# Kernel tuning notes

Hardware: AMD Instinct MI355X
Metric: run time of the kernel (lower is better)

Reference implementation:

```python
import jax, jax.numpy as jnp
import numpy as np

B, S, SEQ_PER = 1, 4, 512            # batch, num_sequences (tickers), per-stock length (seq_len+1)
L = S * SEQ_PER                      # total sequence length = 2048
D_MODEL, NHEAD, HEAD_DIM = 1024, 16, 64
KVC, QC, ROPE = 512, 512, 32
D_FF = 4096
H2 = NHEAD * 2                       # differential attention sub-heads
HD2 = HEAD_DIM // 2
RD2 = ROPE // 2
SCALING = float(((HEAD_DIM + ROPE) // 2) ** -0.5)
LAMBDA_INIT = float(0.8 - 0.6 * np.exp(-0.3 * 0))  # depth = 0
EPS = float(np.finfo(np.float32).eps)              # torch RMSNorm default eps


def rmsnorm(x, w, eps=EPS):
    return x * jax.lax.rsqrt(jnp.mean(x * x, axis=-1, keepdims=True) + eps) * w


def rope_rotate(x, fr, fi):
    # x: (B, S, T, H2, RD2) viewed as complex pairs along last dim; fr/fi: (T, RD2//2)
    a = x[..., 0::2]
    b = x[..., 1::2]
    cr = fr[None, None, :, None, :]
    ci = fi[None, None, :, None, :]
    ya = a * cr - b * ci
    yb = a * ci + b * cr
    return jnp.stack([ya, yb], axis=-1).reshape(x.shape)


def setup_inputs() -> dict:
    key = jax.random.key(0)
    ks = jax.random.split(key, 16)
    x = jax.random.normal(ks[0], (B, L, D_MODEL), dtype=jnp.float32)
    # rotary frequencies for the seq_per_stock-1 rotated positions, rope_dim//4 complex freqs
    t = np.arange(SEQ_PER - 1, dtype=np.float32)
    inv = 1.0 / (10000.0 ** (np.arange(ROPE // 4, dtype=np.float32) / (ROPE // 4)))
    ang = t[:, None] * inv[None, :]
    freqs_r = jnp.asarray(np.cos(ang), dtype=jnp.float32)
    freqs_i = jnp.asarray(np.sin(ang), dtype=jnp.float32)
    # block-tiled causal mask: causal(seq_per) tiled (S,S) -> (1,1,L,L); True = masked
    causal = np.triu(np.ones((SEQ_PER, SEQ_PER), dtype=bool), k=1)
    mask = jnp.asarray(np.tile(causal, (S, S))[None, None])
    w = lambda k, shape: (jax.random.normal(k, shape, dtype=jnp.float32) * 0.02)
    return {
        "x": x, "freqs_r": freqs_r, "freqs_i": freqs_i, "mask": mask,
        "kv_down_w": w(ks[1], (D_MODEL, KVC + ROPE)),
        "q_down_w": w(ks[2], (D_MODEL, QC)),
        "kv_up_w": w(ks[3], (KVC, NHEAD * HEAD_DIM * 2)),
        "q_up_w": w(ks[4], (QC, NHEAD * (HEAD_DIM + ROPE))),
        "kv_norm_w": jnp.ones((KVC,), jnp.float32),
        "q_norm_w": jnp.ones((QC,), jnp.float32),
        "o_w": w(ks[5], (NHEAD * HEAD_DIM, D_MODEL)),
        "lambda_q1": jax.random.normal(ks[6], (HD2,), jnp.float32) * 0.1,
        "lambda_k1": jax.random.normal(ks[7], (HD2,), jnp.float32) * 0.1,
        "lambda_q2": jax.random.normal(ks[8], (HD2,), jnp.float32) * 0.1,
        "lambda_k2": jax.random.normal(ks[9], (HD2,), jnp.float32) * 0.1,
        "head_norm_w": jnp.ones((HEAD_DIM,), jnp.float32),
        "norm1_w": jnp.ones((D_MODEL,), jnp.float32),
        "norm2_w": jnp.ones((D_MODEL,), jnp.float32),
        "ff_in_w": w(ks[10], (D_MODEL, D_FF * 2)),
        "ff_out_w": w(ks[11], (D_FF, D_MODEL)),
    }


def reference(x, freqs_r, freqs_i, mask, kv_down_w, q_down_w, kv_up_w, q_up_w,
              kv_norm_w, q_norm_w, o_w, lambda_q1, lambda_k1, lambda_q2, lambda_k2,
              head_norm_w, norm1_w, norm2_w, ff_in_w, ff_out_w):
    b, sl, _ = x.shape
    # ---- attention sublayer ----
    h = rmsnorm(x, norm1_w)
    ckv = h @ kv_down_w                                   # (B,L,KVC+ROPE)
    c_kv, k_rope = ckv[..., :KVC], ckv[..., KVC:]
    kv = rmsnorm(c_kv, kv_norm_w) @ kv_up_w               # (B,L,NHEAD*HEAD_DIM*2)
    kv = kv.reshape(b, sl, NHEAD, HEAD_DIM * 2)
    k = kv[..., :HEAD_DIM].reshape(b, sl, H2, HD2)
    v = kv[..., HEAD_DIM:]                                # (B,L,NHEAD,HEAD_DIM)
    q_full = rmsnorm(h @ q_down_w, q_norm_w) @ q_up_w
    q_full = q_full.reshape(b, sl, NHEAD, HEAD_DIM + ROPE)
    q = q_full[..., :HEAD_DIM].reshape(b, sl, H2, HD2)
    q_rope = q_full[..., HEAD_DIM:].reshape(b, sl, H2, RD2)
    k_rope = jnp.broadcast_to(k_rope[:, :, None, :], (b, sl, NHEAD, ROPE)).reshape(b, sl, H2, RD2)
    # per-stock RoPE: first token of each stock left unrotated
    qr = q_rope.reshape(b, S, SEQ_PER, H2, RD2)
    kr = k_rope.reshape(b, S, SEQ_PER, H2, RD2)
    q_rot = rope_rotate(qr[:, :, 1:], freqs_r, freqs_i)
    k_rot = rope_rotate(kr[:, :, 1:], freqs_r, freqs_i)
    q_rope = jnp.concatenate([qr[:, :, :1], q_rot], axis=2).reshape(b, sl, H2, RD2)
    k_rope = jnp.concatenate([kr[:, :, :1], k_rot], axis=2).reshape(b, sl, H2, RD2)
    qh = jnp.concatenate([q, q_rope], axis=-1).transpose(0, 2, 1, 3)  # (B,H2,L,HD2+RD2)
    kh = jnp.concatenate([k, k_rope], axis=-1).transpose(0, 2, 1, 3)
    vh = v.transpose(0, 2, 1, 3)                                      # (B,NHEAD,L,HEAD_DIM)
    a = jnp.einsum('bhqd,bhkd->bhqk', qh, kh) * SCALING               # (B,H2,L,L)
    abs_a = jnp.where(mask, -1e9, jnp.abs(a))
    p = jnp.sign(a) * jax.nn.softmax(abs_a, axis=-1)
    lam = (jnp.exp(jnp.sum(lambda_k1 * lambda_q1)) - jnp.exp(jnp.sum(lambda_k2 * lambda_q2))
           + LAMBDA_INIT)
    p = p.reshape(b, NHEAD, 2, sl, sl)
    a1, a2 = p[:, :, 0], p[:, :, 1]
    g = jnp.mean(a1, axis=-2, keepdims=True)                          # (B,NHEAD,1,L)
    attn_w = a1 - lam * a2 + g * lam
    attn_w = jnp.where(mask, 0.0, attn_w)
    out = jnp.einsum('bhqk,bhkd->bhqd', attn_w, vh)                   # (B,NHEAD,L,HEAD_DIM)
    out = rmsnorm(out.transpose(0, 2, 1, 3), head_norm_w, eps=1e-5)
    out = out.reshape(b, sl, NHEAD * HEAD_DIM) @ o_w
    x = x + out
    # ---- SwiGLU FFN sublayer ----
    h2 = rmsnorm(x, norm2_w)
    uv = h2 @ ff_in_w
    u, g2 = uv[..., :D_FF], uv[..., D_FF:]
    x = x + (u * jax.nn.silu(g2)) @ ff_out_w
    return x
```

## Files before the change

kernel.cpp:

```cpp
#include <hip/hip_runtime.h>
#include <math.h>

#define LQ 2048
#define SCALING 0.14433756729740643f
#define FEPS 1.1920928955078125e-07f

typedef unsigned short u16;
typedef __attribute__((ext_vector_type(8))) short bf16x8;
typedef __attribute__((ext_vector_type(4))) float f32x4;

#define MFMA16(a, b, c) __builtin_amdgcn_mfma_f32_16x16x32_bf16((a), (b), (c), 0, 0, 0)

__device__ __forceinline__ u16 f2b(float x) {
  union { float f; unsigned u; } v; v.f = x;
  return (u16)((v.u + 0x7FFFu + ((v.u >> 16) & 1u)) >> 16);
}
__device__ __forceinline__ float b2f(u16 b) {
  union { unsigned u; float f; } v; v.u = ((unsigned)b) << 16;
  return v.f;
}

__global__ __launch_bounds__(256) void prep_weights_kernel(
    const float* __restrict__ kvd, u16* __restrict__ kvd_h, u16* __restrict__ kvd_l,
    const float* __restrict__ qd,  u16* __restrict__ qd_h,  u16* __restrict__ qd_l,
    const float* __restrict__ kvu, u16* __restrict__ kvu_h, u16* __restrict__ kvu_l,
    const float* __restrict__ qu,  u16* __restrict__ qu_h,  u16* __restrict__ qu_l,
    const float* __restrict__ ow,  u16* __restrict__ ow_t,
    const float* __restrict__ ffi, u16* __restrict__ ffi_t,
    const float* __restrict__ ffo, u16* __restrict__ ffo_t) {
  __shared__ float tile[32][33];
  int id = blockIdx.x;
  const float* W; u16* Whi; u16* Wlo = nullptr; int K, N, bx, by;
  if (id < 8192) {
    W = ffi; Whi = ffi_t; K = 1024; N = 8192; bx = id % 256; by = id / 256;
  } else if (id < 8192 + 4096) {
    id -= 8192;
    W = ffo; Whi = ffo_t; K = 4096; N = 1024; bx = id % 32; by = id / 32;
  } else if (id < 12288 + 1024) {
    id -= 12288;
    W = ow; Whi = ow_t; K = 1024; N = 1024; bx = id % 32; by = id / 32;
  } else if (id < 13312 + 544) {
    id -= 13312;
    W = kvd; Whi = kvd_h; Wlo = kvd_l; K = 1024; N = 544; bx = id % 17; by = id / 17;
  } else if (id < 13856 + 512) {
    id -= 13856;
    W = qd; Whi = qd_h; Wlo = qd_l; K = 1024; N = 512; bx = id % 16; by = id / 16;
  } else if (id < 14368 + 1024) {
    id -= 14368;
    W = kvu; Whi = kvu_h; Wlo = kvu_l; K = 512; N = 2048; bx = id % 64; by = id / 64;
  } else {
    id -= 15392;
    W = qu; Whi = qu_h; Wlo = qu_l; K = 512; N = 1536; bx = id % 48; by = id / 48;
  }

  int n0 = bx * 32, k0 = by * 32;
  int tx = threadIdx.x, ty = threadIdx.y;
  for (int i = ty; i < 32; i += 8) {
    int k = k0 + i, n = n0 + tx;
    tile[i][tx] = (k < K && n < N) ? W[(size_t)k * N + n] : 0.f;
  }
  __syncthreads();
  for (int i = ty; i < 32; i += 8) {
    int n = n0 + i, k = k0 + tx;
    if (n < N && k < K) {
      float xv = tile[tx][i];
      u16 hi = f2b(xv);
      Whi[(size_t)n * K + k] = hi;
      if (Wlo) Wlo[(size_t)n * K + k] = f2b(xv - b2f(hi));
    }
  }
}

template <int BF16OUT>
__global__ __launch_bounds__(256) void rmsnorm_kernel(
    const float* __restrict__ x, const float* __restrict__ w, void* __restrict__ outv,
    int cols, int in_stride, float eps) {
  const int row = blockIdx.x;
  const float* xr = x + (size_t)row * in_stride;
  float ss = 0.f;
  for (int c = threadIdx.x; c < cols; c += 256) { float v = xr[c]; ss = fmaf(v, v, ss); }
#pragma unroll
  for (int off = 32; off > 0; off >>= 1) ss += __shfl_xor(ss, off);
  __shared__ float red[4];
  if ((threadIdx.x & 63) == 0) red[threadIdx.x >> 6] = ss;
  __syncthreads();
  float tot = red[0] + red[1] + red[2] + red[3];
  float sc = 1.f / sqrtf(tot / (float)cols + eps);
  for (int c = threadIdx.x; c < cols; c += 256) {
    float v = xr[c] * sc * w[c];
    if (BF16OUT) ((u16*)outv)[(size_t)row * cols + c] = f2b(v);
    else ((float*)outv)[(size_t)row * cols + c] = v;
  }
}

__global__ __launch_bounds__(256) void rmsnorm_split_kernel(
    const float* __restrict__ x, const float* __restrict__ w,
    u16* __restrict__ hi_out, u16* __restrict__ lo_out,
    int cols, int in_stride, float eps) {
  const int row = blockIdx.x;
  const float* xr = x + (size_t)row * in_stride;
  float ss = 0.f;
  for (int c = threadIdx.x; c < cols; c += 256) { float v = xr[c]; ss = fmaf(v, v, ss); }
#pragma unroll
  for (int off = 32; off > 0; off >>= 1) ss += __shfl_xor(ss, off);
  __shared__ float red[4];
  if ((threadIdx.x & 63) == 0) red[threadIdx.x >> 6] = ss;
  __syncthreads();
  float tot = red[0] + red[1] + red[2] + red[3];
  float sc = 1.f / sqrtf(tot / (float)cols + eps);
  for (int c = threadIdx.x; c < cols; c += 256) {
    float v = xr[c] * sc * w[c];
    u16 hi = f2b(v);
    hi_out[(size_t)row * cols + c] = hi;
    lo_out[(size_t)row * cols + c] = f2b(v - b2f(hi));
  }
}

__global__ __launch_bounds__(256) void rmsnorm_split2_kernel(
    const float* __restrict__ in0, const float* __restrict__ w0,
    u16* __restrict__ hi0, u16* __restrict__ lo0, int stride0,
    const float* __restrict__ in1, const float* __restrict__ w1,
    u16* __restrict__ hi1, u16* __restrict__ lo1, int stride1) {
  int row = blockIdx.x;
  const float* xr; const float* w; u16* ho; u16* lo;
  if (row < 2048) {
    xr = in0 + (size_t)row * stride0; w = w0;
    ho = hi0 + (size_t)row * 512; lo = lo0 + (size_t)row * 512;
  } else {
    row -= 2048;
    xr = in1 + (size_t)row * stride1; w = w1;
    ho = hi1 + (size_t)row * 512; lo = lo1 + (size_t)row * 512;
  }
  float ss = 0.f;
  for (int c = threadIdx.x; c < 512; c += 256) { float v = xr[c]; ss = fmaf(v, v, ss); }
#pragma unroll
  for (int off = 32; off > 0; off >>= 1) ss += __shfl_xor(ss, off);
  __shared__ float red[4];
  if ((threadIdx.x & 63) == 0) red[threadIdx.x >> 6] = ss;
  __syncthreads();
  float tot = red[0] + red[1] + red[2] + red[3];
  float sc = 1.f / sqrtf(tot / 512.f + FEPS);
  for (int c = threadIdx.x; c < 512; c += 256) {
    float v = xr[c] * sc * w[c];
    u16 hi = f2b(v);
    ho[c] = hi;
    lo[c] = f2b(v - b2f(hi));
  }
}

__global__ __launch_bounds__(256) void gemm_split(
    const u16* __restrict__ Ahi, const u16* __restrict__ Alo,
    const u16* __restrict__ Bhi, const u16* __restrict__ Blo,
    float* __restrict__ C, int M, int N, int K) {
  __shared__ u16 Ah[64][72];
  __shared__ u16 Al[64][72];
  __shared__ u16 Bh[64][72];
  __shared__ u16 Bl[64][72];

  const int t = threadIdx.x;
  const int lane = t & 63;
  const int wv = t >> 6;
  const int wr = (wv >> 1) * 32;
  const int wc = (wv & 1) * 32;
  const int bm = blockIdx.y * 64;
  const int bn = blockIdx.x * 64;
  const int lr = t >> 2;
  const int lc = (t & 3) * 16;
  const int rsel = lane & 15;
  const int ksel = 8 * (lane >> 4);

  const u16* Ahrow = Ahi + (size_t)(bm + lr) * K + lc;
  const u16* Alrow = Alo + (size_t)(bm + lr) * K + lc;
  const bool bval = (bn + lr) < N;
  const u16* Bhrow = Bhi + (size_t)(bn + lr) * K + lc;
  const u16* Blrow = Blo + (size_t)(bn + lr) * K + lc;

  f32x4 acc[2][2] = {};

  for (int kt = 0; kt < K; kt += 64) {
    uint4 ah0 = *(const uint4*)(Ahrow + kt);
    uint4 ah1 = *(const uint4*)(Ahrow + kt + 8);
    uint4 al0 = *(const uint4*)(Alrow + kt);
    uint4 al1 = *(const uint4*)(Alrow + kt + 8);
    uint4 bh0 = {0, 0, 0, 0}, bh1 = {0, 0, 0, 0}, bl0 = {0, 0, 0, 0}, bl1 = {0, 0, 0, 0};
    if (bval) {
      bh0 = *(const uint4*)(Bhrow + kt); bh1 = *(const uint4*)(Bhrow + kt + 8);
      bl0 = *(const uint4*)(Blrow + kt); bl1 = *(const uint4*)(Blrow + kt + 8);
    }
    __syncthreads();
    *(uint4*)&Ah[lr][lc] = ah0; *(uint4*)&Ah[lr][lc + 8] = ah1;
    *(uint4*)&Al[lr][lc] = al0; *(uint4*)&Al[lr][lc + 8] = al1;
    *(uint4*)&Bh[lr][lc] = bh0; *(uint4*)&Bh[lr][lc + 8] = bh1;
    *(uint4*)&Bl[lr][lc] = bl0; *(uint4*)&Bl[lr][lc + 8] = bl1;
    __syncthreads();
#pragma unroll
    for (int ks = 0; ks < 2; ++ks) {
      const int ko = ks * 32 + ksel;
      bf16x8 a0h = *(const bf16x8*)&Ah[wr + rsel][ko];
      bf16x8 a1h = *(const bf16x8*)&Ah[wr + 16 + rsel][ko];
      bf16x8 a0l = *(const bf16x8*)&Al[wr + rsel][ko];
      bf16x8 a1l = *(const bf16x8*)&Al[wr + 16 + rsel][ko];
      bf16x8 b0h = *(const bf16x8*)&Bh[wc + rsel][ko];
      bf16x8 b1h = *(const bf16x8*)&Bh[wc + 16 + rsel][ko];
      bf16x8 b0l = *(const bf16x8*)&Bl[wc + rsel][ko];
      bf16x8 b1l = *(const bf16x8*)&Bl[wc + 16 + rsel][ko];
      acc[0][0] = MFMA16(a0h, b0h, acc[0][0]);
      acc[0][0] = MFMA16(a0h, b0l, acc[0][0]);
      acc[0][0] = MFMA16(a0l, b0h, acc[0][0]);
      acc[0][1] = MFMA16(a0h, b1h, acc[0][1]);
      acc[0][1] = MFMA16(a0h, b1l, acc[0][1]);
      acc[0][1] = MFMA16(a0l, b1h, acc[0][1]);
      acc[1][0] = MFMA16(a1h, b0h, acc[1][0]);
      acc[1][0] = MFMA16(a1h, b0l, acc[1][0]);
      acc[1][0] = MFMA16(a1l, b0h, acc[1][0]);
      acc[1][1] = MFMA16(a1h, b1h, acc[1][1]);
      acc[1][1] = MFMA16(a1h, b1l, acc[1][1]);
      acc[1][1] = MFMA16(a1l, b1h, acc[1][1]);
    }
  }
  const int r0 = (lane >> 4) * 4;
#pragma unroll
  for (int fm = 0; fm < 2; ++fm)
#pragma unroll
    for (int fn = 0; fn < 2; ++fn)
#pragma unroll
      for (int j = 0; j < 4; ++j) {
        int row = bm + wr + fm * 16 + r0 + j;
        int col = bn + wc + fn * 16 + rsel;
        if (col < N) C[(size_t)row * N + col] = acc[fm][fn][j];
      }
}

template <int GATED, int ADDX>
__global__ __launch_bounds__(256) void gemm_kernel(
    const u16* __restrict__ A, const u16* __restrict__ Bt, const float* __restrict__ X,
    float* __restrict__ C, u16* __restrict__ Cg, int M, int N, int K) {
  __shared__ u16 As[64][72];
  __shared__ u16 Bs[64][72];
  __shared__ u16 Bs2[GATED ? 64 : 1][72];

  const int t = threadIdx.x;
  const int lane = t & 63;
  const int wv = t >> 6;
  const int wr = (wv >> 1) * 32;
  const int wc = (wv & 1) * 32;
  const int bm = blockIdx.y * 64;
  const int bn = blockIdx.x * 64;
  const int lr = t >> 2;
  const int lc = (t & 3) * 16;
  const int rsel = lane & 15;
  const int ksel = 8 * (lane >> 4);

  const u16* Arow = A + (size_t)(bm + lr) * K + lc;
  const u16* Brow = Bt + (size_t)(bn + lr) * K + lc;
  const u16* Brow2 = Bt + (size_t)(4096 + bn + lr) * K + lc;

  f32x4 acc[2][2] = {};
  f32x4 accg[2][2] = {};

  for (int kt = 0; kt < K; kt += 64) {
    uint4 a0 = *(const uint4*)(Arow + kt);
    uint4 a1 = *(const uint4*)(Arow + kt + 8);
    uint4 b0 = *(const uint4*)(Brow + kt);
    uint4 b1 = *(const uint4*)(Brow + kt + 8);
    uint4 c0 = {0, 0, 0, 0}, c1 = {0, 0, 0, 0};
    if (GATED) { c0 = *(const uint4*)(Brow2 + kt); c1 = *(const uint4*)(Brow2 + kt + 8); }
    __syncthreads();
    *(uint4*)&As[lr][lc] = a0; *(uint4*)&As[lr][lc + 8] = a1;
    *(uint4*)&Bs[lr][lc] = b0; *(uint4*)&Bs[lr][lc + 8] = b1;
    if (GATED) { *(uint4*)&Bs2[lr][lc] = c0; *(uint4*)&Bs2[lr][lc + 8] = c1; }
    __syncthreads();
#pragma unroll
    for (int ks = 0; ks < 2; ++ks) {
      const int ko = ks * 32 + ksel;
      bf16x8 af0 = *(const bf16x8*)&As[wr + rsel][ko];
      bf16x8 af1 = *(const bf16x8*)&As[wr + 16 + rsel][ko];
      bf16x8 bf0 = *(const bf16x8*)&Bs[wc + rsel][ko];
      bf16x8 bf1 = *(const bf16x8*)&Bs[wc + 16 + rsel][ko];
      acc[0][0] = MFMA16(af0, bf0, acc[0][0]);
      acc[0][1] = MFMA16(af0, bf1, acc[0][1]);
      acc[1][0] = MFMA16(af1, bf0, acc[1][0]);
      acc[1][1] = MFMA16(af1, bf1, acc[1][1]);
      if (GATED) {
        bf16x8 cf0 = *(const bf16x8*)&Bs2[wc + rsel][ko];
        bf16x8 cf1 = *(const bf16x8*)&Bs2[wc + 16 + rsel][ko];
        accg[0][0] = MFMA16(af0, cf0, accg[0][0]);
        accg[0][1] = MFMA16(af0, cf1, accg[0][1]);
        accg[1][0] = MFMA16(af1, cf0, accg[1][0]);
        accg[1][1] = MFMA16(af1, cf1, accg[1][1]);
      }
    }
  }
  const int r0 = (lane >> 4) * 4;
#pragma unroll
  for (int fm = 0; fm < 2; ++fm)
#pragma unroll
    for (int fn = 0; fn < 2; ++fn)
#pragma unroll
      for (int j = 0; j < 4; ++j) {
        int row = bm + wr + fm * 16 + r0 + j;
        int col = bn + wc + fn * 16 + rsel;
        size_t o = (size_t)row * N + col;
        if (!GATED) {
          float v = acc[fm][fn][j];
          if (ADDX) v += X[o];
          C[o] = v;
        } else {
          float u = acc[fm][fn][j], g = accg[fm][fn][j];
          float sv = g / (1.f + __expf(-g));
          Cg[o] = f2b(u * sv);
        }
      }
}

__global__ __launch_bounds__(256) void build_mid_kernel(
    const float* __restrict__ qfull, const float* __restrict__ kv,
    const float* __restrict__ ckv, const float* __restrict__ fr,
    const float* __restrict__ fi, u16* __restrict__ qhi, u16* __restrict__ qlo,
    u16* __restrict__ khi, u16* __restrict__ klo, u16* __restrict__ vt,
    const float* __restrict__ lq1, const float* __restrict__ lk1,
    const float* __restrict__ lq2, const float* __restrict__ lk2,
    float* __restrict__ lamp) {
  __shared__ u16 tile[64][65];
  int id = blockIdx.x;
  if (id < 16384) {
    const int q = id & 2047;
    const int h2 = ((id >> 11) << 2) + (threadIdx.x >> 6);
    const int d = threadIdx.x & 63;
    const int hh = h2 >> 1, s = h2 & 1;
    const float* row = qfull + (size_t)q * 1536 + hh * 96;
    float val;
    if (d < 32) {
      val = row[s * 32 + d];
    } else if (d < 48) {
      int r = d - 32;
      int pos = q & 511;
      const float* rp = row + 64 + s * 16;
      if (pos == 0) val = rp[r];
      else {
        int j = r >> 1;
        float cr = fr[(pos - 1) * 8 + j], ci = fi[(pos - 1) * 8 + j];
        float a = rp[2 * j], b = rp[2 * j + 1];
        val = (r & 1) ? (a * ci + b * cr) : (a * cr - b * ci);
      }
    } else val = 0.f;
    u16 hi = f2b(val);
    qhi[((size_t)h2 * LQ + q) * 64 + d] = hi;
    qlo[((size_t)h2 * LQ + q) * 64 + d] = f2b(val - b2f(hi));
    return;
  }
  id -= 16384;
  if (id < 16384) {
    const int kp = id & 2047;
    const int h2 = ((id >> 11) << 2) + (threadIdx.x >> 6);
    const int d = threadIdx.x & 63;
    const int hh = h2 >> 1, s = h2 & 1;
    float val;
    if (d < 32) {
      val = kv[(size_t)kp * 2048 + hh * 128 + s * 32 + d];
    } else if (d < 48) {
      int r = d - 32;
      int pos = kp & 511;
      const float* rp = ckv + (size_t)kp * 544 + 512 + s * 16;
      if (pos == 0) val = rp[r];
      else {
        int j = r >> 1;
        float cr = fr[(pos - 1) * 8 + j], ci = fi[(pos - 1) * 8 + j];
        float a = rp[2 * j], b = rp[2 * j + 1];
        val = (r & 1) ? (a * ci + b * cr) : (a * cr - b * ci);
      }
    } else val = 0.f;
    u16 hi = f2b(val);
    khi[((size_t)h2 * LQ + kp) * 64 + d] = hi;
    klo[((size_t)h2 * LQ + kp) * 64 + d] = f2b(val - b2f(hi));
    return;
  }
  id -= 16384;
  if (id < 512) {
    int h = id >> 5, k0 = (id & 31) * 64;
    int t = threadIdx.x;
    int d = t & 63, kr = t >> 6;
#pragma unroll
    for (int i = 0; i < 16; ++i) {
      int k = kr + i * 4;
      tile[k][d] = f2b(kv[(size_t)(k0 + k) * 2048 + h * 128 + 64 + d]);
    }
    __syncthreads();
    int kk = t & 63, dr = t >> 6;
#pragma unroll
    for (int i = 0; i < 16; ++i) {
      int d2 = dr + i * 4;
      vt[((size_t)h * 64 + d2) * LQ + k0 + kk] = tile[kk][d2];
    }
    return;
  }
  int t = threadIdx.x;
  if (t < 32) {
    float a = lq1[t] * lk1[t], b = lq2[t] * lk2[t];
#pragma unroll
    for (int off = 1; off < 32; off <<= 1) { a += __shfl_xor(a, off); b += __shfl_xor(b, off); }
    if (t == 0) lamp[0] = expf(a) - expf(b) + 0.2f;
  }
}

#define SCORE6(z, a0h, a1h, a0l, a1l, ph, pl)                         \
  {                                                                   \
    bf16x8 bh0 = *(const bf16x8*)(ph), bh1 = *(const bf16x8*)((ph) + 32); \
    bf16x8 bl0 = *(const bf16x8*)(pl), bl1 = *(const bf16x8*)((pl) + 32); \
    z = MFMA16(a0h, bh0, z); z = MFMA16(a1h, bh1, z);                 \
    z = MFMA16(a0h, bl0, z); z = MFMA16(a1h, bl1, z);                 \
    z = MFMA16(a0l, bh0, z); z = MFMA16(a1l, bh1, z);                 \
  }

__global__ __launch_bounds__(256) void attn_z_kernel(
    const u16* __restrict__ qhi, const u16* __restrict__ khi,
    float* __restrict__ zp) {
  __shared__ u16 Kh[2][64][72];

  const int bid = blockIdx.x;
  const int c = 7 - (bid >> 9);
  const int r = bid & 511;
  const int h2 = r & 31;
  const int qtIdx = (r >> 5) & 3;
  const int s = r >> 7;
  const int qt = qtIdx * 8 + c;
  const int qb = qt * 64;
  const int t = threadIdx.x;
  const int lane = t & 63, wv = t >> 6;
  const int rsel = lane & 15, grp = lane >> 4, ksel = 8 * grp;
  const int qrow = qb + wv * 16;

  const size_t qoff = ((size_t)h2 * LQ + qrow + rsel) * 64 + ksel;
  bf16x8 aq0h = *(const bf16x8*)(qhi + qoff), aq1h = *(const bf16x8*)(qhi + qoff + 32);
  const u16* kh = khi + (size_t)h2 * LQ * 64;

  const int srow = t >> 2;
  const int scol = (t & 3) * 16;

  int qm[4];
  float Z[4] = {0.f, 0.f, 0.f, 0.f};
#pragma unroll
  for (int j = 0; j < 4; ++j) qm[j] = (qrow + grp * 4 + j) & 511;

  const int kbeg = s * 512;
  int buf = 0;
  for (int jt = 0; jt <= c; ++jt) {
    const int kt = kbeg + jt * 64;
    const size_t kb = (size_t)(kt + srow) * 64 + scol;
    uint4 r0 = *(const uint4*)(kh + kb);
    uint4 r1 = *(const uint4*)(kh + kb + 8);
    *(uint4*)&Kh[buf][srow][scol] = r0;
    *(uint4*)&Kh[buf][srow][scol + 8] = r1;
    __syncthreads();
#pragma unroll
    for (int fk = 0; fk < 4; ++fk) {
      const int krow = fk * 16 + rsel;
      const int k = kt + krow;
      bf16x8 b0 = *(const bf16x8*)&Kh[buf][krow][ksel];
      bf16x8 b1 = *(const bf16x8*)&Kh[buf][krow][ksel + 32];
      f32x4 z = {};
      z = MFMA16(aq0h, b0, z);
      z = MFMA16(aq1h, b1, z);
#pragma unroll
      for (int j = 0; j < 4; ++j)
        if ((k & 511) <= qm[j]) Z[j] += __expf(fabsf(z[j] * SCALING));
    }
    buf ^= 1;
  }
#pragma unroll
  for (int j = 0; j < 4; ++j) {
#pragma unroll
    for (int off = 1; off < 16; off <<= 1) Z[j] += __shfl_xor(Z[j], off);
    if (rsel == 0) {
      int q = qrow + grp * 4 + j;
      zp[((size_t)(s * 32 + h2) << 11) + q] = Z[j];
    }
  }
}

__global__ __launch_bounds__(256) void attn_pv_kernel(
    const u16* __restrict__ qhi, const u16* __restrict__ qlo,
    const u16* __restrict__ khi, const u16* __restrict__ klo,
    const u16* __restrict__ vt, const float* __restrict__ zp,
    const float* __restrict__ lamp,
    float* __restrict__ O0, float* __restrict__ O123, float* __restrict__ colsum) {
  __shared__ u16 KhA[64][72], KlA[64][72], KhB[64][72], KlB[64][72];
  __shared__ u16 Vs[64][72];
  __shared__ u16 pcLDS[4][16][72];
  __shared__ float csLDS[2][4][64];

  const int bid = blockIdx.x;
  const int c = 7 - (bid >> 8);
  const int r = bid & 255;
  const int h = r & 15;
  const int qtIdx = (r >> 4) & 3;
  const int s = r >> 6;
  const int qt = qtIdx * 8 + c;
  const int qb = qt * 64;
  const int t = threadIdx.x;
  const int lane = t & 63, wv = t >> 6;
  const int rsel = lane & 15, grp = lane >> 4, ksel = 8 * grp;
  const int qrow = qb + wv * 16;
  const float lam = lamp[0];

  const int h2a = 2 * h, h2b = 2 * h + 1;
  const size_t qoffa = ((size_t)h2a * LQ + qrow + rsel) * 64 + ksel;
  const size_t qoffb = ((size_t)h2b * LQ + qrow + rsel) * 64 + ksel;
  bf16x8 aqa0h = *(const bf16x8*)(qhi + qoffa), aqa1h = *(const bf16x8*)(qhi + qoffa + 32);
  bf16x8 aqa0l = *(const bf16x8*)(qlo + qoffa), aqa1l = *(const bf16x8*)(qlo + qoffa + 32);
  bf16x8 aqb0h = *(const bf16x8*)(qhi + qoffb), aqb1h = *(const bf16x8*)(qhi + qoffb + 32);
  bf16x8 aqb0l = *(const bf16x8*)(qlo + qoffb), aqb1l = *(const bf16x8*)(qlo + qoffb + 32);
  const u16* kha = khi + (size_t)h2a * LQ * 64;
  const u16* kla = klo + (size_t)h2a * LQ * 64;
  const u16* khb = khi + (size_t)h2b * LQ * 64;
  const u16* klb = klo + (size_t)h2b * LQ * 64;
  const u16* vb = vt + (size_t)h * 64 * LQ;

  const int srow = t >> 2;
  const int scol = (t & 3) * 16;

  int qm[4];
  float iz1[4], iz2[4];
#pragma unroll
  for (int j = 0; j < 4; ++j) {
    int q = qrow + grp * 4 + j;
    qm[j] = q & 511;
    float z1 = 0.f, z2 = 0.f;
#pragma unroll
    for (int ss = 0; ss < 4; ++ss) {
      z1 += zp[((size_t)(ss * 32 + h2a) << 11) + q];
      z2 += zp[((size_t)(ss * 32 + h2b) << 11) + q];
    }
    iz1[j] = 1.f / z1;
    iz2[j] = 1.f / z2;
  }

  f32x4 accO[4] = {};
  const int kbeg = s * 512;
  int buf = 0;

  for (int jt = c + 1; jt < 8; ++jt) {
    if (t < 64) colsum[((size_t)h * 32 + qt) * LQ + kbeg + jt * 64 + t] = 0.f;
  }

  uint4 rha0, rha1, rla0, rla1, rhb0, rhb1, rlb0, rlb1, rv0, rv1;
  {
    const size_t kb = (size_t)(kbeg + srow) * 64 + scol;
    rha0 = *(const uint4*)(kha + kb);
    rha1 = *(const uint4*)(kha + kb + 8);
    rla0 = *(const uint4*)(kla + kb);
    rla1 = *(const uint4*)(kla + kb + 8);
    rhb0 = *(const uint4*)(khb + kb);
    rhb1 = *(const uint4*)(khb + kb + 8);
    rlb0 = *(const uint4*)(klb + kb);
    rlb1 = *(const uint4*)(klb + kb + 8);
    const u16* vsrc = vb + (size_t)srow * LQ + kbeg + scol;
    rv0 = *(const uint4*)(vsrc);
    rv1 = *(const uint4*)(vsrc + 8);
  }

  for (int jt = 0; jt <= c; ++jt) {
    const int kt = kbeg + jt * 64;

    *(uint4*)&KhA[srow][scol] = rha0; *(uint4*)&KhA[srow][scol + 8] = rha1;
    *(uint4*)&KlA[srow][scol] = rla0; *(uint4*)&KlA[srow][scol + 8] = rla1;
    *(uint4*)&KhB[srow][scol] = rhb0; *(uint4*)&KhB[srow][scol + 8] = rhb1;
    *(uint4*)&KlB[srow][scol] = rlb0; *(uint4*)&KlB[srow][scol + 8] = rlb1;
    *(uint4*)&Vs[srow][scol] = rv0;  *(uint4*)&Vs[srow][scol + 8] = rv1;
    __syncthreads();

    if (jt < c) {
      const size_t kb = (size_t)(kt + 64 + srow) * 64 + scol;
      rha0 = *(const uint4*)(kha + kb);
      rha1 = *(const uint4*)(kha + kb + 8);
      rla0 = *(const uint4*)(kla + kb);
      rla1 = *(const uint4*)(kla + kb + 8);
      rhb0 = *(const uint4*)(khb + kb);
      rhb1 = *(const uint4*)(khb + kb + 8);
      rlb0 = *(const uint4*)(klb + kb);
      rlb1 = *(const uint4*)(klb + kb + 8);
      const u16* vsrc = vb + (size_t)srow * LQ + kt + 64 + scol;
      rv0 = *(const uint4*)(vsrc);
      rv1 = *(const uint4*)(vsrc + 8);
    }

    __builtin_amdgcn_s_setprio(1);
    float pc[4][4], cs[4];
#pragma unroll
    for (int fk = 0; fk < 4; ++fk) {
      const int krow = fk * 16 + rsel;
      const int k = kt + krow;
      f32x4 z = {};
      SCORE6(z, aqa0h, aqa1h, aqa0l, aqa1l, &KhA[krow][ksel], &KlA[krow][ksel]);
      f32x4 w = {};
      SCORE6(w, aqb0h, aqb1h, aqb0l, aqb1l, &KhB[krow][ksel], &KlB[krow][ksel]);
      float csj = 0.f;
#pragma unroll
      for (int j = 0; j < 4; ++j) {
        bool msk = ((k & 511) > qm[j]);
        float sa = z[j] * SCALING;
        float pa = __builtin_copysignf(__expf(fabsf(sa)) * iz1[j], sa);
        pa = msk ? 0.f : pa;
        csj += pa;
        float sb = w[j] * SCALING;
        float pb = __builtin_copysignf(__expf(fabsf(sb)) * iz2[j], sb);
        pc[fk][j] = pa - (msk ? 0.f : lam * pb);
      }
      cs[fk] = csj;
    }
#pragma unroll
    for (int fk = 0; fk < 4; ++fk)
#pragma unroll
      for (int j = 0; j < 4; ++j)
        pcLDS[wv][grp * 4 + j][fk * 16 + rsel] = f2b(pc[fk][j]);
#pragma unroll
    for (int kc = 0; kc < 2; ++kc) {
      bf16x8 ap = *(const bf16x8*)&pcLDS[wv][rsel][kc * 32 + ksel];
#pragma unroll
      for (int fn = 0; fn < 4; ++fn) {
        bf16x8 bv = *(const bf16x8*)&Vs[fn * 16 + rsel][kc * 32 + ksel];
        accO[fn] = MFMA16(ap, bv, accO[fn]);
      }
    }
    __builtin_amdgcn_s_setprio(0);
#pragma unroll
    for (int fk = 0; fk < 4; ++fk) {
      float cc = cs[fk];
      cc += __shfl_xor(cc, 16);
      cc += __shfl_xor(cc, 32);
      if (grp == 0) csLDS[buf][wv][fk * 16 + rsel] = cc;
    }
    __syncthreads();
    if (t < 64) {
      float tot = csLDS[buf][0][t] + csLDS[buf][1][t] + csLDS[buf][2][t] + csLDS[buf][3][t];
      colsum[((size_t)h * 32 + qt) * LQ + kt + t] = tot;
    }
    buf ^= 1;
  }
  float* Op = (s == 0) ? O0 : (O123 + (size_t)(s - 1) * 16 * LQ * 64);
#pragma unroll
  for (int fn = 0; fn < 4; ++fn)
#pragma unroll
    for (int j = 0; j < 4; ++j) {
      int q = qrow + grp * 4 + j;
      int d = fn * 16 + rsel;
      Op[((size_t)h * LQ + q) * 64 + d] = accO[fn][j];
    }
}

__global__ void g_reduce_kernel(const float* __restrict__ colsum, float* __restrict__ g) {
  int idx = blockIdx.x * 256 + threadIdx.x;
  if (idx >= 16 * LQ) return;
  int h = idx >> 11, k = idx & 2047;
  float s = 0.f;
#pragma unroll
  for (int qt = 0; qt < 32; ++qt) s += colsum[((size_t)h * 32 + qt) * LQ + k];
  g[idx] = s * (1.f / 2048.f);
}

__global__ __launch_bounds__(512) void gv_wscan_kernel(const float* __restrict__ g,
                                                       const u16* __restrict__ vt,
                                                       float* __restrict__ W) {
  __shared__ float s[512];
  int h = blockIdx.x >> 6, d = blockIdx.x & 63;
  int t = threadIdx.x;
  float v = 0.f;
#pragma unroll
  for (int seg = 0; seg < 4; ++seg) {
    int k = seg * 512 + t;
    v += g[h * 2048 + k] * b2f(vt[((size_t)h * 64 + d) * LQ + k]);
  }
  s[t] = v;
  __syncthreads();
  for (int off = 1; off < 512; off <<= 1) {
    float add = (t >= off) ? s[t - off] : 0.f;
    __syncthreads();
    s[t] += add;
    __syncthreads();
  }
  W[((size_t)h * 512 + t) * 64 + d] = s[t];
}

__global__ __launch_bounds__(256) void combine_norm_kernel(
    const float* __restrict__ O0, const float* __restrict__ O123,
    const float* __restrict__ W, const float* __restrict__ hw,
    const float* __restrict__ lamp, u16* __restrict__ out) {
  const int q = blockIdx.x;
  const int h = blockIdx.y * 4 + (threadIdx.x >> 6);
  const int d = threadIdx.x & 63;
  const float lam = lamp[0];
  const size_t S = (size_t)16 * LQ * 64;
  const size_t idx = ((size_t)h * LQ + q) * 64 + d;
  float v = O0[idx] + O123[idx] + O123[idx + S] + O123[idx + 2 * S] +
            lam * W[((size_t)h * 512 + (q & 511)) * 64 + d];
  float ss = v * v;
#pragma unroll
  for (int off = 1; off < 64; off <<= 1) ss += __shfl_xor(ss, off);
  float sc = 1.f / sqrtf(ss * (1.f / 64.f) + 1e-5f);
  out[(size_t)q * 1024 + h * 64 + d] = f2b(v * sc * hw[d]);
}

extern "C" void kernel_launch(void* const* d_in, const int* in_sizes, int n_in,
                              void* d_out, int out_size, void* d_ws, size_t ws_size,
                              hipStream_t stream) {
  const float* x = (const float*)d_in[0];
  const float* freqs_r = (const float*)d_in[1];
  const float* freqs_i = (const float*)d_in[2];
  const float* kv_down_w = (const float*)d_in[4];
  const float* q_down_w = (const float*)d_in[5];
  const float* kv_up_w = (const float*)d_in[6];
  const float* q_up_w = (const float*)d_in[7];
  const float* kv_norm_w = (const float*)d_in[8];
  const float* q_norm_w = (const float*)d_in[9];
  const float* o_w = (const float*)d_in[10];
  const float* lambda_q1 = (const float*)d_in[11];
  const float* lambda_k1 = (const float*)d_in[12];
  const float* lambda_q2 = (const float*)d_in[13];
  const float* lambda_k2 = (const float*)d_in[14];
  const float* head_norm_w = (const float*)d_in[15];
  const float* norm1_w = (const float*)d_in[16];
  const float* norm2_w = (const float*)d_in[17];
  const float* ff_in_w = (const float*)d_in[18];
  const float* ff_out_w = (const float*)d_in[19];
  float* out = (float*)d_out;
  char* ws = (char*)d_ws;

  const size_t WT_KVD_H = 0;
  const size_t WT_KVD_L = WT_KVD_H + (size_t)544 * 1024 * 2;
  const size_t WT_QD_H  = WT_KVD_L + (size_t)544 * 1024 * 2;
  const size_t WT_QD_L  = WT_QD_H + (size_t)512 * 1024 * 2;
  const size_t WT_KVU_H = WT_QD_L + (size_t)512 * 1024 * 2;
  const size_t WT_KVU_L = WT_KVU_H + (size_t)2048 * 512 * 2;
  const size_t WT_QU_H  = WT_KVU_L + (size_t)2048 * 512 * 2;
  const size_t WT_QU_L  = WT_QU_H + (size_t)1536 * 512 * 2;
  const size_t WT_OW    = WT_QU_L + (size_t)1536 * 512 * 2;
  const size_t WT_FFI   = WT_OW + (size_t)1024 * 1024 * 2;
  const size_t WT_FFO   = WT_FFI + (size_t)8192 * 1024 * 2;
  const size_t A0 = WT_FFO + (size_t)1024 * 4096 * 2;

  const size_t H     = A0;
  const size_t CKV   = A0 + 8388608;
  const size_t CKVN  = A0 + 12845056;
  const size_t KVB   = A0 + 17039360;
  const size_t CQ    = A0 + 33816576;
  const size_t CQN   = A0 + 38010880;
  const size_t QFULL = A0 + 42205184;
  const size_t QHI = H;
  const size_t KHI = QFULL;
  const size_t KLO = A0 + 50593792;
  const size_t QLO = A0 + 58982400;
  const size_t VT  = CKVN;
  const size_t OP0   = 0;
  const size_t OP123 = KVB;
  const size_t CS  = CKV;
  const size_t GB  = A0 + 67371008;
  const size_t GV  = A0 + 67502080;
  const size_t WB  = A0 + 69599232;
  const size_t LAM = A0 + 71696384;
  const size_t ZP  = A0 + 71696640;
  const size_t WS_END = A0 + 72745216;
  const size_t ATTN  = CKV;
  const size_t X1    = KVB + 8388608;
  const size_t H2N   = H;
  const size_t FFACT = QFULL;

  if (ws_size < WS_END) return;

  u16* wt_kvd_h = (u16*)(ws + WT_KVD_H); u16* wt_kvd_l = (u16*)(ws + WT_KVD_L);
  u16* wt_qd_h  = (u16*)(ws + WT_QD_H);  u16* wt_qd_l  = (u16*)(ws + WT_QD_L);
  u16* wt_kvu_h = (u16*)(ws + WT_KVU_H); u16* wt_kvu_l = (u16*)(ws + WT_KVU_L);
  u16* wt_qu_h  = (u16*)(ws + WT_QU_H);  u16* wt_qu_l  = (u16*)(ws + WT_QU_L);
  u16* wt_ow  = (u16*)(ws + WT_OW);
  u16* wt_ffi = (u16*)(ws + WT_FFI);
  u16* wt_ffo = (u16*)(ws + WT_FFO);
  u16* h_hi   = (u16*)(ws + H);
  u16* h_lo   = (u16*)(ws + H + 4194304);
  float* ckv  = (float*)(ws + CKV);
  u16* ckvn_hi = (u16*)(ws + CKVN);
  u16* ckvn_lo = (u16*)(ws + CKVN + 2097152);
  float* kvb  = (float*)(ws + KVB);
  float* cq   = (float*)(ws + CQ);
  u16* cqn_hi = (u16*)(ws + CQN);
  u16* cqn_lo = (u16*)(ws + CQN + 2097152);
  float* qfull = (float*)(ws + QFULL);
  u16* qhib = (u16*)(ws + QHI); u16* qlob = (u16*)(ws + QLO);
  u16* khib = (u16*)(ws + KHI); u16* klob = (u16*)(ws + KLO);
  u16* vtb  = (u16*)(ws + VT);
  float* zpb = (float*)(ws + ZP);
  float* Op0 = (float*)(ws + OP0);
  float* Op123 = (float*)(ws + OP123);
  float* csb = (float*)(ws + CS);
  float* gb  = (float*)(ws + GB);
  float* wbb = (float*)(ws + WB);
  float* lamp = (float*)(ws + LAM);
  u16* attn_n = (u16*)(ws + ATTN);
  float* x1 = (float*)(ws + X1);
  u16* h2n = (u16*)(ws + H2N);
  u16* ffact = (u16*)(ws + FFACT);

  prep_weights_kernel<<<16160, dim3(32, 8), 0, stream>>>(
      kv_down_w, wt_kvd_h, wt_kvd_l, q_down_w, wt_qd_h, wt_qd_l,
      kv_up_w, wt_kvu_h, wt_kvu_l, q_up_w, wt_qu_h, wt_qu_l,
      o_w, wt_ow, ff_in_w, wt_ffi, ff_out_w, wt_ffo);

  rmsnorm_split_kernel<<<2048, 256, 0, stream>>>(x, norm1_w, h_hi, h_lo, 1024, 1024, FEPS);
  gemm_split<<<dim3(9, 32), 256, 0, stream>>>(h_hi, h_lo, wt_kvd_h, wt_kvd_l, ckv,
                                              2048, 544, 1024);
  gemm_split<<<dim3(8, 32), 256, 0, stream>>>(h_hi, h_lo, wt_qd_h, wt_qd_l, cq,
                                              2048, 512, 1024);
  rmsnorm_split2_kernel<<<4096, 256, 0, stream>>>(ckv, kv_norm_w, ckvn_hi, ckvn_lo, 544,
                                                  cq, q_norm_w, cqn_hi, cqn_lo, 512);
  gemm_split<<<dim3(32, 32), 256, 0, stream>>>(ckvn_hi, ckvn_lo, wt_kvu_h, wt_kvu_l, kvb,
                                               2048, 2048, 512);
  gemm_split<<<dim3(24, 32), 256, 0, stream>>>(cqn_hi, cqn_lo, wt_qu_h, wt_qu_l, qfull,
                                               2048, 1536, 512);

  build_mid_kernel<<<33281, 256, 0, stream>>>(qfull, kvb, ckv, freqs_r, freqs_i,
                                              qhib, qlob, khib, klob, vtb,
                                              lambda_q1, lambda_k1, lambda_q2, lambda_k2,
                                              lamp);

  attn_z_kernel<<<4096, 256, 0, stream>>>(qhib, khib, zpb);
  attn_pv_kernel<<<2048, 256, 0, stream>>>(qhib, qlob, khib, klob, vtb, zpb,
                                           lamp, Op0, Op123, csb);

  g_reduce_kernel<<<128, 256, 0, stream>>>(csb, gb);
  gv_wscan_kernel<<<1024, 512, 0, stream>>>(gb, vtb, wbb);
  combine_norm_kernel<<<dim3(2048, 4), 256, 0, stream>>>(Op0, Op123, wbb, head_norm_w,
                                                         lamp, attn_n);

  gemm_kernel<0, 1><<<dim3(16, 32), 256, 0, stream>>>(attn_n, wt_ow, x, x1, nullptr,
                                                      2048, 1024, 1024);
  rmsnorm_kernel<1><<<2048, 256, 0, stream>>>(x1, norm2_w, h2n, 1024, 1024, FEPS);
  gemm_kernel<1, 0><<<dim3(64, 32), 256, 0, stream>>>(h2n, wt_ffi, nullptr, nullptr, ffact,
                                                      2048, 4096, 1024);
  gemm_kernel<0, 1><<<dim3(16, 32), 256, 0, stream>>>(ffact, wt_ffo, x1, out, nullptr,
                                                      2048, 1024, 4096);
}
```

Baseline: 355.5 us.

## Fold first RMSNorm into weight prep and add 128-row gated FFN GEMM

Appends 2048 extra blocks to the weight-prep kernel that compute the first RMSNorm hi/lo split, removing a separate launch. Replaces the gated SwiGLU up-projection GEMM with a new kernel using 128x64 tiles, where each wave computes 32 rows against both the u and gate weight tiles. This doubles A-tile reuse per block and halves the grid size. It also raises register use per thread, which may lower occupancy.

```diff
diff --git a/kernel.cpp b/kernel.cpp
--- a/kernel.cpp
+++ b/kernel.cpp
@@ -27,9 +27,34 @@
     const float* __restrict__ qu,  u16* __restrict__ qu_h,  u16* __restrict__ qu_l,
     const float* __restrict__ ow,  u16* __restrict__ ow_t,
     const float* __restrict__ ffi, u16* __restrict__ ffi_t,
-    const float* __restrict__ ffo, u16* __restrict__ ffo_t) {
+    const float* __restrict__ ffo, u16* __restrict__ ffo_t,
+    const float* __restrict__ x, const float* __restrict__ norm1_w,
+    u16* __restrict__ h_hi, u16* __restrict__ h_lo) {
   __shared__ float tile[32][33];
+  __shared__ float red[4];
   int id = blockIdx.x;
+
+  if (id >= 16160) {
+    const int row = id - 16160;
+    const int tid = threadIdx.y * 32 + threadIdx.x;
+    const float* xr = x + (size_t)row * 1024;
+    float ss = 0.f;
+    for (int c = tid; c < 1024; c += 256) { float v = xr[c]; ss = fmaf(v, v, ss); }
+#pragma unroll
+    for (int off = 32; off > 0; off >>= 1) ss += __shfl_xor(ss, off);
+    if ((tid & 63) == 0) red[tid >> 6] = ss;
+    __syncthreads();
+    float tot = red[0] + red[1] + red[2] + red[3];
+    float sc = 1.f / sqrtf(tot / 1024.f + FEPS);
+    for (int c = tid; c < 1024; c += 256) {
+      float v = xr[c] * sc * norm1_w[c];
+      u16 hi = f2b(v);
+      h_hi[(size_t)row * 1024 + c] = hi;
+      h_lo[(size_t)row * 1024 + c] = f2b(v - b2f(hi));
+    }
+    return;
+  }
+
   const float* W; u16* Whi; u16* Wlo = nullptr; int K, N, bx, by;
   if (id < 8192) {
     W = ffi; Whi = ffi_t; K = 1024; N = 8192; bx = id % 256; by = id / 256;
@@ -90,29 +115,6 @@
     float v = xr[c] * sc * w[c];
     if (BF16OUT) ((u16*)outv)[(size_t)row * cols + c] = f2b(v);
     else ((float*)outv)[(size_t)row * cols + c] = v;
-  }
-}
-
-__global__ __launch_bounds__(256) void rmsnorm_split_kernel(
-    const float* __restrict__ x, const float* __restrict__ w,
-    u16* __restrict__ hi_out, u16* __restrict__ lo_out,
-    int cols, int in_stride, float eps) {
-  const int row = blockIdx.x;
-  const float* xr = x + (size_t)row * in_stride;
-  float ss = 0.f;
-  for (int c = threadIdx.x; c < cols; c += 256) { float v = xr[c]; ss = fmaf(v, v, ss); }
-#pragma unroll
-  for (int off = 32; off > 0; off >>= 1) ss += __shfl_xor(ss, off);
-  __shared__ float red[4];
-  if ((threadIdx.x & 63) == 0) red[threadIdx.x >> 6] = ss;
-  __syncthreads();
-  float tot = red[0] + red[1] + red[2] + red[3];
-  float sc = 1.f / sqrtf(tot / (float)cols + eps);
-  for (int c = threadIdx.x; c < cols; c += 256) {
-    float v = xr[c] * sc * w[c];
-    u16 hi = f2b(v);
-    hi_out[(size_t)row * cols + c] = hi;
-    lo_out[(size_t)row * cols + c] = f2b(v - b2f(hi));
   }
 }
 
@@ -310,6 +312,88 @@
           float sv = g / (1.f + __expf(-g));
           Cg[o] = f2b(u * sv);
         }
+      }
+}
+
+__global__ __launch_bounds__(256) void gemm_m128_gated(
+    const u16* __restrict__ A, const u16* __restrict__ Bt,
+    u16* __restrict__ Cg, int M, int N, int K) {
+  __shared__ u16 As[128][72];
+  __shared__ u16 Bs[64][72];
+  __shared__ u16 Bs2[64][72];
+
+  const int t = threadIdx.x;
+  const int lane = t & 63;
+  const int wv = t >> 6;
+  const int wr = wv * 32;
+  const int bm = blockIdx.y * 128;
+  const int bn = blockIdx.x * 64;
+  const int lr = t >> 2;
+  const int lc = (t & 3) * 16;
+  const int rsel = lane & 15;
+  const int ksel = 8 * (lane >> 4);
+
+  const u16* Arow0 = A + (size_t)(bm + lr) * K + lc;
+  const u16* Arow1 = A + (size_t)(bm + 64 + lr) * K + lc;
+  const u16* Brow = Bt + (size_t)(bn + lr) * K + lc;
+  const u16* Brow2 = Bt + (size_t)(4096 + bn + lr) * K + lc;
+
+  f32x4 acc[2][4] = {};
+  f32x4 accg[2][4] = {};
+
+  for (int kt = 0; kt < K; kt += 64) {
+    uint4 a00 = *(const uint4*)(Arow0 + kt);
+    uint4 a01 = *(const uint4*)(Arow0 + kt + 8);
+    uint4 a10 = *(const uint4*)(Arow1 + kt);
+    uint4 a11 = *(const uint4*)(Arow1 + kt + 8);
+    uint4 b0 = *(const uint4*)(Brow + kt);
+    uint4 b1 = *(const uint4*)(Brow + kt + 8);
+    uint4 c0 = *(const uint4*)(Brow2 + kt);
+    uint4 c1 = *(const uint4*)(Brow2 + kt + 8);
+    __syncthreads();
+    *(uint4*)&As[lr][lc] = a00; *(uint4*)&As[lr][lc + 8] = a01;
+    *(uint4*)&As[64 + lr][lc] = a10; *(uint4*)&As[64 + lr][lc + 8] = a11;
+    *(uint4*)&Bs[lr][lc] = b0; *(uint4*)&Bs[lr][lc + 8] = b1;
+    *(uint4*)&Bs2[lr][lc] = c0; *(uint4*)&Bs2[lr][lc + 8] = c1;
+    __syncthreads();
+#pragma unroll
+    for (int ks = 0; ks < 2; ++ks) {
+      const int ko = ks * 32 + ksel;
+      bf16x8 af0 = *(const bf16x8*)&As[wr + rsel][ko];
+      bf16x8 af1 = *(const bf16x8*)&As[wr + 16 + rsel][ko];
+      bf16x8 bf[4];
+#pragma unroll
+      for (int fn = 0; fn < 4; ++fn)
+        bf[fn] = *(const bf16x8*)&Bs[fn * 16 + rsel][ko];
+#pragma unroll
+      for (int fn = 0; fn < 4; ++fn) {
+        acc[0][fn] = MFMA16(af0, bf[fn], acc[0][fn]);
+        acc[1][fn] = MFMA16(af1, bf[fn], acc[1][fn]);
+      }
+      bf16x8 cf[4];
+#pragma unroll
+      for (int fn = 0; fn < 4; ++fn)
+        cf[fn] = *(const bf16x8*)&Bs2[fn * 16 + rsel][ko];
+#pragma unroll
+      for (int fn = 0; fn < 4; ++fn) {
+        accg[0][fn] = MFMA16(af0, cf[fn], accg[0][fn]);
+        accg[1][fn] = MFMA16(af1, cf[fn], accg[1][fn]);
+      }
+    }
+  }
+  const int r0 = (lane >> 4) * 4;
+#pragma unroll
+  for (int fm = 0; fm < 2; ++fm)
+#pragma unroll
+    for (int fn = 0; fn < 4; ++fn)
+#pragma unroll
+      for (int j = 0; j < 4; ++j) {
+        int row = bm + wr * 0 + wv * 32 + fm * 16 + r0 + j;
+        int col = bn + fn * 16 + rsel;
+        size_t o = (size_t)row * N + col;
+        float u = acc[fm][fn][j], g = accg[fm][fn][j];
+        float sv = g / (1.f + __expf(-g));
+        Cg[o] = f2b(u * sv);
       }
 }
 
@@ -754,7 +838,6 @@
   const size_t OP123 = KVB;
   const size_t CS  = CKV;
   const size_t GB  = A0 + 67371008;
-  const size_t GV  = A0 + 67502080;
   const size_t WB  = A0 + 69599232;
   const size_t LAM = A0 + 71696384;
   const size_t ZP  = A0 + 71696640;
@@ -798,12 +881,12 @@
   u16* h2n = (u16*)(ws + H2N);
   u16* ffact = (u16*)(ws + FFACT);
 
-  prep_weights_kernel<<<16160, dim3(32, 8), 0, stream>>>(
+  prep_weights_kernel<<<18208, dim3(32, 8), 0, stream>>>(
       kv_down_w, wt_kvd_h, wt_kvd_l, q_down_w, wt_qd_h, wt_qd_l,
       kv_up_w, wt_kvu_h, wt_kvu_l, q_up_w, wt_qu_h, wt_qu_l,
-      o_w, wt_ow, ff_in_w, wt_ffi, ff_out_w, wt_ffo);
-
-  rmsnorm_split_kernel<<<2048, 256, 0, stream>>>(x, norm1_w, h_hi, h_lo, 1024, 1024, FEPS);
+      o_w, wt_ow, ff_in_w, wt_ffi, ff_out_w, wt_ffo,
+      x, norm1_w, h_hi, h_lo);
+
   gemm_split<<<dim3(9, 32), 256, 0, stream>>>(h_hi, h_lo, wt_kvd_h, wt_kvd_l, ckv,
                                               2048, 544, 1024);
   gemm_split<<<dim3(8, 32), 256, 0, stream>>>(h_hi, h_lo, wt_qd_h, wt_qd_l, cq,
@@ -832,8 +915,7 @@
   gemm_kernel<0, 1><<<dim3(16, 32), 256, 0, stream>>>(attn_n, wt_ow, x, x1, nullptr,
                                                       2048, 1024, 1024);
   rmsnorm_kernel<1><<<2048, 256, 0, stream>>>(x1, norm2_w, h2n, 1024, 1024, FEPS);
-  gemm_kernel<1, 0><<<dim3(64, 32), 256, 0, stream>>>(h2n, wt_ffi, nullptr, nullptr, ffact,
-                                                      2048, 4096, 1024);
+  gemm_m128_gated<<<dim3(64, 16), 256, 0, stream>>>(h2n, wt_ffi, ffact, 2048, 4096, 1024);
   gemm_kernel<0, 1><<<dim3(16, 32), 256, 0, stream>>>(ffact, wt_ffo, x1, out, nullptr,
                                                       2048, 1024, 4096);
 }
```

Result: no change. 351.9 us (-1.0%).
